# Kernel tuning notes

Measured on AMD Instinct MI355X. Metric: run time of the kernel, lower is better.

## Reference

```python
import jax, jax.numpy as jnp
import numpy as np

T = 2048; HIDDEN = 2048; HQ = 32; G = 2; D = 64
KERNEL = 32; STRIDE = 16; BLOCK = 64; TOPK = 16
INIT_BLOCKS = 1; LOCAL_BLOCKS = 2; WINDOW = 512
ROPE_BASE = 10000.0
NEG = -1e30


def _rope(x):
    # x: [T, H, D], non-interleaved rotate-half rope
    t, h, d = x.shape
    half = d // 2
    inv = 1.0 / (ROPE_BASE ** (jnp.arange(half, dtype=jnp.float32) / half))
    freqs = jnp.arange(t, dtype=jnp.float32)[:, None] * inv[None, :]
    cos = jnp.cos(freqs)[:, None, :]
    sin = jnp.sin(freqs)[:, None, :]
    x1, x2 = x[..., :half], x[..., half:]
    return jnp.concatenate([x1 * cos - x2 * sin, x2 * cos + x1 * sin], axis=-1)


def setup_inputs() -> dict:
    key = jax.random.key(0)
    ks = jax.random.split(key, 8)
    s = 0.02
    return {
        "hidden_states": jax.random.normal(ks[0], (1, T, HIDDEN), jnp.float32),
        "Wq": jax.random.normal(ks[1], (HQ * D, HIDDEN), jnp.float32) * s,
        "Wk": jax.random.normal(ks[2], (G * D, HIDDEN), jnp.float32) * s,
        "Wv": jax.random.normal(ks[3], (G * D, HIDDEN), jnp.float32) * s,
        "Wo": jax.random.normal(ks[4], (HIDDEN, HQ * D), jnp.float32) * s,
        "Wgate": jax.random.normal(ks[5], (3, HIDDEN), jnp.float32) * s,
        "compress_key": jax.random.normal(ks[6], (G, D * KERNEL, D), jnp.float32) * s,
        "compress_value": jax.random.normal(ks[7], (G, D * KERNEL, D), jnp.float32) * s,
    }


def reference(hidden_states, Wq, Wk, Wv, Wo, Wgate, compress_key, compress_value):
    x = hidden_states[0]                      # [T, HIDDEN] (single varlen sequence)
    scale = 1.0 / np.sqrt(D).astype(np.float32)
    q = (x @ Wq.T).reshape(T, HQ, D)
    k = (x @ Wk.T).reshape(T, G, D)
    v = (x @ Wv.T).reshape(T, G, D)
    gate = jax.nn.sigmoid(x @ Wgate.T)        # [T, 3]
    q = _rope(q)
    k = _rope(k)

    # --- branch 1: compressed attention (linear_compress + compressed_attention) ---
    C = (T - KERNEL) // STRIDE + 1            # compressed sequence length
    starts = jnp.arange(C) * STRIDE
    win_idx = starts[:, None] + jnp.arange(KERNEL)[None, :]        # [C, KERNEL]
    kw = k[win_idx].transpose(2, 0, 1, 3).reshape(G, C, KERNEL * D)
    vw = v[win_idx].transpose(2, 0, 1, 3).reshape(G, C, KERNEL * D)
    ck = jnp.einsum('gcf,gfd->cgd', kw, compress_key)              # [C, G, D]
    cv = jnp.einsum('gcf,gfd->cgd', vw, compress_value)

    qg = q.reshape(T, G, HQ // G, D)          # [T, G, group, D]
    cs = jnp.einsum('tghd,cgd->ghtc', qg, ck) * scale              # [G, grp, T, C]
    # query i may attend compressed token j iff i >= j*stride + kernel - 1
    cmask = jnp.arange(T)[:, None] >= (starts + KERNEL - 1)[None, :]  # [T, C]
    cs = jnp.where(cmask[None, None], cs, NEG)
    p = jax.nn.softmax(cs, axis=-1)
    valid = cmask.any(-1)                     # queries with >=1 compressed key
    p = jnp.where(valid[None, None, :, None], p, 0.0)
    comp_out = jnp.einsum('ghtc,cgd->tghd', p, cv).reshape(T, HQ, D)

    # --- topk block selection from pooled compressed attention scores ---
    NB = T // BLOCK
    bstart = jnp.arange(NB) * BLOCK
    # compressed token j overlaps key block b
    overlap = ((starts[:, None] < bstart[None, :] + BLOCK) &
               (starts[:, None] + KERNEL > bstart[None, :])).astype(p.dtype)  # [C, NB]
    score = jnp.einsum('ghtc,cb->gtb', p, overlap)                 # [G, T, NB]
    qblock = jnp.arange(T) // BLOCK
    b = jnp.arange(NB)
    causal_b = b[None, :] <= qblock[:, None]                       # [T, NB]
    forced = (b[None, :] < INIT_BLOCKS) | (((qblock[:, None] - b[None, :]) < LOCAL_BLOCKS) & causal_b)
    score = jnp.where(forced[None], jnp.inf, score)
    score = jnp.where(causal_b[None], score, -jnp.inf)
    _, topk_idx = jax.lax.top_k(score, TOPK)                       # [G, T, TOPK]
    tk_valid = jnp.take_along_axis(score, topk_idx, axis=-1) > -jnp.inf
    sel = ((topk_idx[..., None] == b) & tk_valid[..., None]).any(axis=2)  # [G, T, NB]

    # --- branch 2: topk block-sparse attention ---
    key_block = jnp.arange(T) // BLOCK
    keymask = sel[:, :, key_block]                                 # [G, T, Tk]
    causal = jnp.arange(T)[:, None] >= jnp.arange(T)[None, :]      # [T, Tk]
    smask = keymask & causal[None]
    ss = jnp.einsum('tghd,sgd->ghts', qg, k) * scale               # [G, grp, T, Tk]
    ss = jnp.where(smask[:, None], ss, NEG)
    sparse_out = jnp.einsum('ghts,sgd->tghd', jax.nn.softmax(ss, -1), v).reshape(T, HQ, D)

    # --- branch 3: sliding window attention (causal, left window) ---
    delta = jnp.arange(T)[:, None] - jnp.arange(T)[None, :]
    wmask = (delta >= 0) & (delta <= WINDOW)                       # [T, Tk]
    ws = jnp.einsum('tghd,sgd->ghts', qg, k) * scale
    ws = jnp.where(wmask[None, None], ws, NEG)
    slide_out = jnp.einsum('ghts,sgd->tghd', jax.nn.softmax(ws, -1), v).reshape(T, HQ, D)

    # --- learned gate fusion + output projection ---
    out = (gate[:, 0, None, None] * comp_out +
           gate[:, 1, None, None] * sparse_out +
           gate[:, 2, None, None] * slide_out)                    # [T, HQ, D]
    o = out.reshape(T, HQ * D) @ Wo.T
    return o[None]                                                 # [1, T, HIDDEN]
```

## Files before the change

### kernel.cpp

```cpp
#include <hip/hip_runtime.h>
#include <math.h>

#define T_SEQ 2048
#define NHQ 32
#define NG 2
#define HD 64
#define CSTRIDE 16
#define KVGW 384

typedef __attribute__((ext_vector_type(8))) short short8_t;
typedef __attribute__((ext_vector_type(4))) short short4_t;
typedef __attribute__((ext_vector_type(4))) float f32x4;

__device__ __forceinline__ ushort f2bf(float x) {
  union { float f; unsigned u; } c; c.f = x;
  unsigned r = c.u + 0x7fff + ((c.u >> 16) & 1);
  return (ushort)(r >> 16);
}
__device__ __forceinline__ float bf2f(ushort u) {
  union { unsigned u; float f; } c; c.u = ((unsigned)u) << 16;
  return c.f;
}

__device__ __forceinline__ void glds16(const ushort* g, ushort* l) {
  __builtin_amdgcn_global_load_lds(
      (const __attribute__((address_space(1))) unsigned int*)g,
      (__attribute__((address_space(3))) unsigned int*)l, 16, 0, 0);
}

__global__ __launch_bounds__(512) void mgemm(
    const ushort* __restrict__ A, const ushort* __restrict__ B,
    float* __restrict__ C, int M, int N, int K) {
  __shared__ __align__(16) ushort As[128 * 64];
  __shared__ __align__(16) ushort Bs[128 * 64];
  const int tid = threadIdx.x;
  const int lane = tid & 63, w = tid >> 6;
  const int quad = lane >> 4, l16 = lane & 15;
  const int m0 = blockIdx.y * 128, n0 = blockIdx.x * 128;
  const int mq = (w & 1) * 64, nq = (w >> 1) * 32;
  f32x4 acc[4][2];
  const f32x4 fz = {0.f, 0.f, 0.f, 0.f};
  #pragma unroll
  for (int i = 0; i < 4; ++i)
    #pragma unroll
    for (int j = 0; j < 2; ++j) acc[i][j] = fz;

  for (int k0 = 0; k0 < K; k0 += 64) {
    __syncthreads();
    #pragma unroll
    for (int j = 0; j < 2; ++j) {
      int ci = j * 512 + tid;
      int row = ci >> 3, cl = ci & 7;
      int kc = cl ^ (row & 7);
      glds16(A + ((size_t)(m0 + row) * K + k0 + kc * 8), &As[ci * 8]);
      glds16(B + ((size_t)(n0 + row) * K + k0 + kc * 8), &Bs[ci * 8]);
    }
    __syncthreads();
    #pragma unroll
    for (int kt = 0; kt < 2; ++kt) {
      short8_t af[4], bf_[2];
      #pragma unroll
      for (int mt = 0; mt < 4; ++mt) {
        int row = mq + mt * 16 + l16;
        int cl = (kt * 4 + quad) ^ (row & 7);
        af[mt] = *(const short8_t*)&As[row * 64 + cl * 8];
      }
      #pragma unroll
      for (int nt = 0; nt < 2; ++nt) {
        int row = nq + nt * 16 + l16;
        int cl = (kt * 4 + quad) ^ (row & 7);
        bf_[nt] = *(const short8_t*)&Bs[row * 64 + cl * 8];
      }
      #pragma unroll
      for (int mt = 0; mt < 4; ++mt)
        #pragma unroll
        for (int nt = 0; nt < 2; ++nt)
          acc[mt][nt] = __builtin_amdgcn_mfma_f32_16x16x32_bf16(
              af[mt], bf_[nt], acc[mt][nt], 0, 0, 0);
    }
  }
  #pragma unroll
  for (int mt = 0; mt < 4; ++mt)
    #pragma unroll
    for (int nt = 0; nt < 2; ++nt)
      #pragma unroll
      for (int r = 0; r < 4; ++r) {
        int m = m0 + mq + mt * 16 + quad * 4 + r;
        int n = n0 + nq + nt * 16 + l16;
        C[(size_t)m * N + n] = acc[mt][nt][r];
      }
}

__global__ __launch_bounds__(256) void cvt_bf(const float* __restrict__ src,
                                              ushort* __restrict__ dst, int n) {
  int i = blockIdx.x * 256 + threadIdx.x;
  if (i < n) dst[i] = f2bf(src[i]);
}

__global__ __launch_bounds__(256) void cvt_sum2_bf(const float* __restrict__ a,
                                                   const float* __restrict__ b,
                                                   ushort* __restrict__ dst, int n) {
  int i = blockIdx.x * 256 + threadIdx.x;
  if (i < n) dst[i] = f2bf(a[i] + b[i]);
}

__global__ __launch_bounds__(256) void pack_wkvg(
    const float* __restrict__ Wk, const float* __restrict__ Wv,
    const float* __restrict__ Wg, ushort* __restrict__ dst) {
  int i = blockIdx.x * 256 + threadIdx.x;
  if (i >= KVGW * 2048) return;
  int n = i >> 11, k = i & 2047;
  float v;
  if (n < 128) v = Wk[(size_t)n * 2048 + k];
  else if (n < 256) v = Wv[(size_t)(n - 128) * 2048 + k];
  else if (n < 259) v = Wg[(size_t)(n - 256) * 2048 + k];
  else v = 0.f;
  dst[i] = f2bf(v);
}

__global__ __launch_bounds__(256) void cvt_vt(const float* __restrict__ kvg,
                                              ushort* __restrict__ vt) {
  int i = blockIdx.x * 256 + threadIdx.x;
  if (i >= T_SEQ * NG * HD) return;
  int d = i & 63, g = (i >> 6) & 1, s = i >> 7;
  int blk = s >> 6, k = s & 63;
  int snew = blk * 64 + (((k >> 2) ^ (d & 15)) << 2) + (k & 3);
  vt[((size_t)g * HD + d) * T_SEQ + snew] =
      f2bf(kvg[(size_t)s * KVGW + 128 + g * 64 + d]);
}

__global__ __launch_bounds__(256) void rope_all(
    const float* __restrict__ q, float* __restrict__ kvg,
    ushort* __restrict__ qbf, ushort* __restrict__ kbf) {
  const int t = blockIdx.x;
  const float lnb_over = 9.210340371976184f / 32.f;
  for (int job = threadIdx.x; job < (NHQ + NG) * 32; job += 256) {
    int h = job >> 5, j = job & 31;
    float inv = expf(-(float)j * lnb_over);
    float fr = (float)t * inv;
    float c_ = cosf(fr), s_ = sinf(fr);
    if (h < NHQ) {
      const float cq = c_ * 0.125f, sq = s_ * 0.125f;
      const float* base = q + ((size_t)t * NHQ + h) * HD;
      float x1 = base[j], x2 = base[j + 32];
      ushort* ob = qbf + ((size_t)t * NHQ + h) * HD;
      ob[j] = f2bf(x1 * cq - x2 * sq);
      ob[j + 32] = f2bf(x2 * cq + x1 * sq);
    } else {
      int g = h - NHQ;
      float* base = kvg + (size_t)t * KVGW + g * 64;
      float x1 = base[j], x2 = base[j + 32];
      float o1 = x1 * c_ - x2 * s_, o2 = x2 * c_ + x1 * s_;
      base[j] = o1; base[j + 32] = o2;
      kbf[(size_t)t * 128 + g * 64 + j] = f2bf(o1);
      kbf[(size_t)t * 128 + g * 64 + j + 32] = f2bf(o2);
    }
  }
}

__global__ __launch_bounds__(256) void compress_kv(
    const float* __restrict__ kvg,
    const float* __restrict__ Wck, const float* __restrict__ Wcv,
    ushort* __restrict__ ck16, ushort* __restrict__ cvt16) {
  const int c = blockIdx.x, g = blockIdx.y;
  const int tid = threadIdx.x;
  if (c == 127) {
    if (tid < 64) ck16[((size_t)127 * NG + g) * HD + tid] = 0;
    else if (tid < 128) cvt16[((size_t)g * HD + (tid - 64)) * 128 + 127] = 0;
    return;
  }
  const int d = tid & 63, chunk = tid >> 6;
  __shared__ float red[2][4][64];
  float ak = 0.f, av = 0.f;
  for (int f = chunk * 512; f < chunk * 512 + 512; ++f) {
    int i = f >> 6, e = f & 63;
    int trow = c * CSTRIDE + i;
    float kv = kvg[(size_t)trow * KVGW + g * 64 + e];
    float vv = kvg[(size_t)trow * KVGW + 128 + g * 64 + e];
    ak += kv * Wck[((size_t)g * 2048 + f) * HD + d];
    av += vv * Wcv[((size_t)g * 2048 + f) * HD + d];
  }
  red[0][chunk][d] = ak;
  red[1][chunk][d] = av;
  __syncthreads();
  if (tid < 64) {
    ck16[((size_t)c * NG + g) * HD + tid] =
        f2bf(red[0][0][tid] + red[0][1][tid] + red[0][2][tid] + red[0][3][tid]);
  } else if (tid < 128) {
    int dd = tid - 64;
    cvt16[((size_t)g * HD + dd) * 128 + c] =
        f2bf(red[1][0][dd] + red[1][1][dd] + red[1][2][dd] + red[1][3][dd]);
  }
}

__global__ __launch_bounds__(512) void comp_attn(
    const ushort* __restrict__ qbf, const ushort* __restrict__ ck16,
    const ushort* __restrict__ cvt16, const float* __restrict__ kvg,
    float* __restrict__ comb, unsigned* __restrict__ sel) {
  const int tb = blockIdx.x, g = blockIdx.y;
  const int t0 = tb * 16;
  const int tid = threadIdx.x, lane = tid & 63, w = tid >> 6;
  const int quad = lane >> 4, l16 = lane & 15;
  const int qb = t0 >> 6;

  __shared__ float colsum[16][129];
  for (int i = tid; i < 16 * 129; i += 512) ((float*)colsum)[i] = 0.f;
  __syncthreads();

  const int t = t0 + l16;
  const int cmaxv = (t >= 31) ? min(126, (t - 31) >> 4) : -1;
  const int h0 = w * 2;

  short8_t qB[2][2];
  #pragma unroll
  for (int hh = 0; hh < 2; ++hh)
    #pragma unroll
    for (int kd = 0; kd < 2; ++kd)
      qB[hh][kd] = *(const short8_t*)(qbf +
          ((size_t)t * NHQ + g * 16 + h0 + hh) * HD + kd * 32 + quad * 8);

  const f32x4 fz = {0.f, 0.f, 0.f, 0.f};
  f32x4 sp[2][8];

  #pragma unroll
  for (int ct = 0; ct < 8; ++ct) {
    const ushort* kr = ck16 + ((size_t)(ct * 16 + l16) * NG + g) * HD + quad * 8;
    short8_t kA0 = *(const short8_t*)kr;
    short8_t kA1 = *(const short8_t*)(kr + 32);
    #pragma unroll
    for (int hh = 0; hh < 2; ++hh) {
      f32x4 c0 = __builtin_amdgcn_mfma_f32_16x16x32_bf16(kA0, qB[hh][0], fz, 0, 0, 0);
      sp[hh][ct] = __builtin_amdgcn_mfma_f32_16x16x32_bf16(kA1, qB[hh][1], c0, 0, 0, 0);
    }
  }

  short4_t pB[2][8];
  #pragma unroll
  for (int hh = 0; hh < 2; ++hh) {
    float mx = -INFINITY;
    #pragma unroll
    for (int ct = 0; ct < 8; ++ct)
      #pragma unroll
      for (int r = 0; r < 4; ++r) {
        int c = ct * 16 + quad * 4 + r;
        float s_ = (c <= cmaxv) ? sp[hh][ct][r] : -INFINITY;
        sp[hh][ct][r] = s_;
        mx = fmaxf(mx, s_);
      }
    mx = fmaxf(mx, __shfl_xor(mx, 16));
    mx = fmaxf(mx, __shfl_xor(mx, 32));
    if (mx == -INFINITY) mx = 0.f;
    float ls = 0.f;
    #pragma unroll
    for (int ct = 0; ct < 8; ++ct)
      #pragma unroll
      for (int r = 0; r < 4; ++r) {
        float p = __expf(sp[hh][ct][r] - mx);
        sp[hh][ct][r] = p;
        ls += p;
      }
    ls += __shfl_xor(ls, 16);
    ls += __shfl_xor(ls, 32);
    float inv = (ls > 0.f) ? 1.f / ls : 0.f;
    #pragma unroll
    for (int ct = 0; ct < 8; ++ct) {
      short4_t pk;
      #pragma unroll
      for (int r = 0; r < 4; ++r) {
        float pn = sp[hh][ct][r] * inv;
        sp[hh][ct][r] = pn;
        pk[r] = (short)f2bf(pn);
      }
      pB[hh][ct] = pk;
    }
  }

  #pragma unroll
  for (int ct = 0; ct < 8; ++ct)
    #pragma unroll
    for (int r = 0; r < 4; ++r)
      atomicAdd(&colsum[l16][ct * 16 + quad * 4 + r],
                sp[0][ct][r] + sp[1][ct][r]);

  f32x4 acc[2][4];
  #pragma unroll
  for (int hh = 0; hh < 2; ++hh)
    #pragma unroll
    for (int dt = 0; dt < 4; ++dt) acc[hh][dt] = fz;
  #pragma unroll
  for (int ct = 0; ct < 8; ++ct) {
    short4_t vA[4];
    #pragma unroll
    for (int dt = 0; dt < 4; ++dt)
      vA[dt] = *(const short4_t*)(cvt16 +
          ((size_t)g * HD + dt * 16 + l16) * 128 + ct * 16 + quad * 4);
    #pragma unroll
    for (int hh = 0; hh < 2; ++hh)
      #pragma unroll
      for (int dt = 0; dt < 4; ++dt)
        acc[hh][dt] = __builtin_amdgcn_mfma_f32_16x16x16bf16_1k(
            vA[dt], pB[hh][ct], acc[hh][dt], 0, 0, 0);
  }

  const float g0 = 1.f / (1.f + __expf(-kvg[(size_t)t * KVGW + 256]));
  #pragma unroll
  for (int hh = 0; hh < 2; ++hh)
    #pragma unroll
    for (int dt = 0; dt < 4; ++dt)
      #pragma unroll
      for (int r = 0; r < 4; ++r)
        comb[((size_t)t * NHQ + g * 16 + h0 + hh) * HD + dt * 16 + quad * 4 + r] =
            g0 * acc[hh][dt][r];

  __syncthreads();

  {
    const int tl = tid >> 5;
    const int b = tid & 31;
    float s;
    if (b > qb) s = -INFINITY;
    else if (b == 0 || qb - b < 2) s = INFINITY;
    else {
      s = 0.f;
      #pragma unroll
      for (int i = 0; i < 5; ++i) s += colsum[tl][4 * b - 1 + i];
    }
    unsigned key = (s < 0.f) ? 0u : (__float_as_uint(s) + 1u);
    unsigned msel = 0;
    for (int it = 0; it < 16; ++it) {
      unsigned long long pk =
          (((unsigned long long)key) << 6) | (unsigned)(63 - b);
      #pragma unroll
      for (int off = 16; off >= 1; off >>= 1) {
        unsigned long long o = __shfl_xor(pk, off);
        if (o > pk) pk = o;
      }
      if ((pk >> 6) == 0) break;
      int bs = 63 - (int)(pk & 63);
      msel |= 1u << bs;
      if (b == bs) key = 0;
    }
    if (b == 0) sel[(size_t)(t0 + tl) * NG + g] = msel;
  }
}

__global__ __launch_bounds__(512, 2) void mfma_attn(
    const ushort* __restrict__ qb16, const ushort* __restrict__ kb16,
    const ushort* __restrict__ vtb, const float* __restrict__ kvg,
    const unsigned* __restrict__ sel, float* __restrict__ comb1,
    float* __restrict__ comb2) {
  const int qb = blockIdx.x, g = blockIdx.y;
  const int hgp = blockIdx.z & 7, mode = blockIdx.z >> 3;
  const int tid = threadIdx.x, lane = tid & 63, w = tid >> 6;
  const int quad = lane >> 4, l16 = lane & 15;
  const int head = g * 16 + hgp * 2 + (w >> 2);
  const int t0 = qb * 64;

  __shared__ __align__(16) ushort Ks[2][64 * 64];
  __shared__ __align__(16) ushort Vs[2][64 * 64];
  __shared__ unsigned sel_s[64];

  if (tid < 64) sel_s[tid] = sel[(size_t)(t0 + tid) * NG + g];
  __syncthreads();

  const int qg = t0 + (w & 3) * 16 + l16;
  const unsigned sbq = sel_s[(w & 3) * 16 + l16];

  short8_t qB0 = *(const short8_t*)(qb16 +
      ((size_t)qg * NHQ + head) * HD + quad * 8);
  short8_t qB1 = *(const short8_t*)(qb16 +
      ((size_t)qg * NHQ + head) * HD + 32 + quad * 8);

  float m_ = -1e30f;
  f32x4 acc[4], accL;
  const f32x4 fz = {0.f, 0.f, 0.f, 0.f};
  #pragma unroll
  for (int dt = 0; dt < 4; ++dt) acc[dt] = fz;
  accL = fz;
  const short4_t onesA = {(short)0x3F80, (short)0x3F80,
                          (short)0x3F80, (short)0x3F80};

  unsigned mrem = 0; int b0 = 0, nb = 0;
  if (mode == 0) {
    unsigned uni = sel_s[lane];
    #pragma unroll
    for (int off = 32; off >= 1; off >>= 1) uni |= __shfl_xor(uni, off);
    mrem = uni;
    nb = __popc(mrem);
  } else {
    b0 = (qb > 8) ? qb - 8 : 0;
    nb = qb - b0 + 1;
  }

  #define STAGE(buf, blk)                                                     \
    {                                                                         \
      const int blk_ = (blk);                                                 \
      const int row = tid >> 3, cl = tid & 7;                                 \
      const int kck = cl ^ (row & 7);                                         \
      glds16(kb16 + (size_t)(blk_ * 64 + row) * 128 + g * 64 + kck * 8,       \
             &Ks[buf][tid * 8]);                                              \
      glds16(vtb + ((size_t)g * 64 + row) * 2048 + blk_ * 64 + cl * 8,        \
             &Vs[buf][tid * 8]);                                              \
    }

  int blkcur;
  if (mode == 0) { blkcur = __ffs(mrem) - 1; mrem &= mrem - 1; }
  else blkcur = b0;
  STAGE(0, blkcur);
  __syncthreads();

  const int e = l16 & 7;

  for (int ib = 0; ib < nb; ++ib) {
    const int cur = ib & 1;
    const int blk = blkcur;
    if (ib + 1 < nb) {
      if (mode == 0) { blkcur = __ffs(mrem) - 1; mrem &= mrem - 1; }
      else blkcur = b0 + ib + 1;
      STAGE(cur ^ 1, blkcur);
    }

    f32x4 sp[4];
    __builtin_amdgcn_s_setprio(1);
    #pragma unroll
    for (int kt = 0; kt < 4; ++kt) {
      const ushort* kr = &Ks[cur][(kt * 16 + l16) * 64];
      short8_t kA0 = *(const short8_t*)(kr + ((quad ^ e) * 8));
      short8_t kA1 = *(const short8_t*)(kr + ((quad ^ e ^ 4) * 8));
      f32x4 c = __builtin_amdgcn_mfma_f32_16x16x32_bf16(kA0, qB0, fz, 0, 0, 0);
      sp[kt] = __builtin_amdgcn_mfma_f32_16x16x32_bf16(kA1, qB1, c, 0, 0, 0);
    }
    __builtin_amdgcn_s_setprio(0);

    const bool diag = (blk == qb);
    const bool wedge = (mode == 1) && (blk == qb - 8);
    const bool selq = (mode != 0) || (((sbq >> blk) & 1u) != 0);

    float mx = -INFINITY;
    if (!diag && !wedge) {
      #pragma unroll
      for (int kt = 0; kt < 4; ++kt)
        #pragma unroll
        for (int r = 0; r < 4; ++r) {
          float s_ = selq ? sp[kt][r] : -INFINITY;
          sp[kt][r] = s_;
          mx = fmaxf(mx, s_);
        }
    } else {
      #pragma unroll
      for (int kt = 0; kt < 4; ++kt)
        #pragma unroll
        for (int r = 0; r < 4; ++r) {
          int key = blk * 64 + kt * 16 + quad * 4 + r;
          bool ok = selq && (key <= qg) && (qg - key <= 512);
          float s_ = ok ? sp[kt][r] : -INFINITY;
          sp[kt][r] = s_;
          mx = fmaxf(mx, s_);
        }
    }
    mx = fmaxf(mx, __shfl_xor(mx, 16));
    mx = fmaxf(mx, __shfl_xor(mx, 32));
    float mold = m_;
    if (!__all(mx <= mold + 8.f)) {
      float mnew = fmaxf(mold, mx);
      float alpha = __expf(mold - mnew);
      #pragma unroll
      for (int dt = 0; dt < 4; ++dt)
        #pragma unroll
        for (int r = 0; r < 4; ++r) acc[dt][r] *= alpha;
      #pragma unroll
      for (int r = 0; r < 4; ++r) accL[r] *= alpha;
      m_ = mnew;
      mold = mnew;
    }
    short4_t pB[4];
    #pragma unroll
    for (int kt = 0; kt < 4; ++kt) {
      float p0 = __expf(sp[kt][0] - mold);
      float p1 = __expf(sp[kt][1] - mold);
      float p2 = __expf(sp[kt][2] - mold);
      float p3 = __expf(sp[kt][3] - mold);
      union { unsigned u[2]; short4_t s; } pk;
      asm("v_cvt_pk_bf16_f32 %0, %1, %2" : "=v"(pk.u[0]) : "v"(p0), "v"(p1));
      asm("v_cvt_pk_bf16_f32 %0, %1, %2" : "=v"(pk.u[1]) : "v"(p2), "v"(p3));
      pB[kt] = pk.s;
    }

    __builtin_amdgcn_s_setprio(1);
    #pragma unroll
    for (int kt = 0; kt < 4; ++kt) {
      #pragma unroll
      for (int dt = 0; dt < 4; ++dt) {
        short4_t vA = *(const short4_t*)(&Vs[cur][(dt * 16 + l16) * 64 +
                                                  (((kt * 4 + quad) ^ l16) << 2)]);
        acc[dt] = __builtin_amdgcn_mfma_f32_16x16x16bf16_1k(
            vA, pB[kt], acc[dt], 0, 0, 0);
      }
      accL = __builtin_amdgcn_mfma_f32_16x16x16bf16_1k(
          onesA, pB[kt], accL, 0, 0, 0);
    }
    __builtin_amdgcn_s_setprio(0);

    __syncthreads();
  }
  #undef STAGE

  const float l_ = accL[0];
  const float c_ =
      (1.f / (1.f + __expf(-kvg[(size_t)qg * KVGW + 257 + mode]))) / l_;
  #pragma unroll
  for (int dt = 0; dt < 4; ++dt)
    #pragma unroll
    for (int r = 0; r < 4; ++r) {
      const int d = dt * 16 + quad * 4 + r;
      size_t idx = ((size_t)qg * NHQ + head) * HD + d;
      if (mode == 0) comb1[idx] += c_ * acc[dt][r];
      else           comb2[idx]  = c_ * acc[dt][r];
    }
}

extern "C" void kernel_launch(void* const* d_in, const int* in_sizes, int n_in,
                              void* d_out, int out_size, void* d_ws, size_t ws_size,
                              hipStream_t stream) {
  const float* x   = (const float*)d_in[0];
  const float* Wq  = (const float*)d_in[1];
  const float* Wk  = (const float*)d_in[2];
  const float* Wv  = (const float*)d_in[3];
  const float* Wo  = (const float*)d_in[4];
  const float* Wg  = (const float*)d_in[5];
  const float* Wck = (const float*)d_in[6];
  const float* Wcv = (const float*)d_in[7];
  float* out = (float*)d_out;
  float* ws = (float*)d_ws;

  float* qbuf   = ws;
  float* comb1  = qbuf + 4194304;
  float* kvg    = comb1 + 4194304;
  float* ckb    = kvg + 786432;
  float* cvb    = ckb + 16384;
  unsigned* sel = (unsigned*)(cvb + 16384);
  ushort* kbf   = (ushort*)(sel + 4096);
  ushort* vtb   = kbf + 262144;
  ushort* wkvgb = vtb + 262144;
  ushort* regA  = wkvgb + 786432;
  ushort* regB  = regA + 4194304;
  ushort* xb = regA;      ushort* combb = regA;
  ushort* wqb = regB;     ushort* qbf = regB;
  float* comb2 = qbuf;
  ushort* wob = (ushort*)qbuf;

  ushort* ckb16 = (ushort*)ckb;
  ushort* cvtb  = ckb16 + 16384;

  const int CV = (4194304 + 255) / 256;
  cvt_bf<<<CV, 256, 0, stream>>>(x, xb, 4194304);
  cvt_bf<<<CV, 256, 0, stream>>>(Wq, wqb, 4194304);
  pack_wkvg<<<(KVGW * 2048 + 255) / 256, 256, 0, stream>>>(Wk, Wv, Wg, wkvgb);

  mgemm<<<dim3(16, 16), 512, 0, stream>>>(xb, wqb, qbuf, 2048, 2048, 2048);
  mgemm<<<dim3(3, 16), 512, 0, stream>>>(xb, wkvgb, kvg, 2048, KVGW, 2048);

  rope_all<<<2048, 256, 0, stream>>>(qbuf, kvg, qbf, kbf);
  cvt_vt<<<(262144 + 255) / 256, 256, 0, stream>>>(kvg, vtb);
  compress_kv<<<dim3(128, 2), 256, 0, stream>>>(kvg, Wck, Wcv, ckb16, cvtb);
  comp_attn<<<dim3(128, 2), 512, 0, stream>>>(qbf, ckb16, cvtb, kvg, comb1, sel);
  mfma_attn<<<dim3(32, 2, 16), 512, 0, stream>>>(qbf, kbf, vtb, kvg, sel, comb1, comb2);

  cvt_sum2_bf<<<CV, 256, 0, stream>>>(comb1, comb2, combb, 4194304);
  cvt_bf<<<CV, 256, 0, stream>>>(Wo, wob, 4194304);
  mgemm<<<dim3(16, 16), 512, 0, stream>>>(combb, wob, out, 2048, 2048, 2048);
}
```

Before: 399.5 us.

## Shrink GEMM tile to 128x64, vectorize conversions, reverse attention block order

The GEMM kernel now uses 256-thread blocks with 128x64 output tiles, doubling the grid so more blocks fill the CUs, though each block reuses less data. The fp32-to-bf16 conversion kernels now process four elements per thread with float4 loads and short4 stores, cutting instruction count per element. Both attention kernels launch query blocks in reverse order, so the longer causal blocks start first and load balance improves. Together these are unrelated tweaks touching several kernels.

```diff
diff --git a/kernel.cpp b/kernel.cpp
--- a/kernel.cpp
+++ b/kernel.cpp
@@ -28,15 +28,15 @@
       (__attribute__((address_space(3))) unsigned int*)l, 16, 0, 0);
 }
 
-__global__ __launch_bounds__(512) void mgemm(
+__global__ __launch_bounds__(256) void mgemm(
     const ushort* __restrict__ A, const ushort* __restrict__ B,
     float* __restrict__ C, int M, int N, int K) {
   __shared__ __align__(16) ushort As[128 * 64];
-  __shared__ __align__(16) ushort Bs[128 * 64];
+  __shared__ __align__(16) ushort Bs[64 * 64];
   const int tid = threadIdx.x;
   const int lane = tid & 63, w = tid >> 6;
   const int quad = lane >> 4, l16 = lane & 15;
-  const int m0 = blockIdx.y * 128, n0 = blockIdx.x * 128;
+  const int m0 = blockIdx.y * 128, n0 = blockIdx.x * 64;
   const int mq = (w & 1) * 64, nq = (w >> 1) * 32;
   f32x4 acc[4][2];
   const f32x4 fz = {0.f, 0.f, 0.f, 0.f};
@@ -48,11 +48,17 @@
   for (int k0 = 0; k0 < K; k0 += 64) {
     __syncthreads();
     #pragma unroll
-    for (int j = 0; j < 2; ++j) {
-      int ci = j * 512 + tid;
+    for (int j = 0; j < 4; ++j) {
+      int ci = j * 256 + tid;
       int row = ci >> 3, cl = ci & 7;
       int kc = cl ^ (row & 7);
       glds16(A + ((size_t)(m0 + row) * K + k0 + kc * 8), &As[ci * 8]);
+    }
+    #pragma unroll
+    for (int j = 0; j < 2; ++j) {
+      int ci = j * 256 + tid;
+      int row = ci >> 3, cl = ci & 7;
+      int kc = cl ^ (row & 7);
       glds16(B + ((size_t)(n0 + row) * K + k0 + kc * 8), &Bs[ci * 8]);
     }
     __syncthreads();
@@ -93,15 +99,24 @@
 
 __global__ __launch_bounds__(256) void cvt_bf(const float* __restrict__ src,
                                               ushort* __restrict__ dst, int n) {
-  int i = blockIdx.x * 256 + threadIdx.x;
-  if (i < n) dst[i] = f2bf(src[i]);
+  int i = (blockIdx.x * 256 + threadIdx.x) * 4;
+  if (i >= n) return;
+  float4 v = *(const float4*)(src + i);
+  short4_t o = {(short)f2bf(v.x), (short)f2bf(v.y),
+                (short)f2bf(v.z), (short)f2bf(v.w)};
+  *(short4_t*)(dst + i) = o;
 }
 
 __global__ __launch_bounds__(256) void cvt_sum2_bf(const float* __restrict__ a,
                                                    const float* __restrict__ b,
                                                    ushort* __restrict__ dst, int n) {
-  int i = blockIdx.x * 256 + threadIdx.x;
-  if (i < n) dst[i] = f2bf(a[i] + b[i]);
+  int i = (blockIdx.x * 256 + threadIdx.x) * 4;
+  if (i >= n) return;
+  float4 va = *(const float4*)(a + i);
+  float4 vb = *(const float4*)(b + i);
+  short4_t o = {(short)f2bf(va.x + vb.x), (short)f2bf(va.y + vb.y),
+                (short)f2bf(va.z + vb.z), (short)f2bf(va.w + vb.w)};
+  *(short4_t*)(dst + i) = o;
 }
 
 __global__ __launch_bounds__(256) void pack_wkvg(
@@ -197,7 +212,7 @@
     const ushort* __restrict__ qbf, const ushort* __restrict__ ck16,
     const ushort* __restrict__ cvt16, const float* __restrict__ kvg,
     float* __restrict__ comb, unsigned* __restrict__ sel) {
-  const int tb = blockIdx.x, g = blockIdx.y;
+  const int tb = 127 - blockIdx.x, g = blockIdx.y;
   const int t0 = tb * 16;
   const int tid = threadIdx.x, lane = tid & 63, w = tid >> 6;
   const int quad = lane >> 4, l16 = lane & 15;
@@ -349,7 +364,7 @@
     const ushort* __restrict__ vtb, const float* __restrict__ kvg,
     const unsigned* __restrict__ sel, float* __restrict__ comb1,
     float* __restrict__ comb2) {
-  const int qb = blockIdx.x, g = blockIdx.y;
+  const int qb = 31 - blockIdx.x, g = blockIdx.y;
   const int hgp = blockIdx.z & 7, mode = blockIdx.z >> 3;
   const int tid = threadIdx.x, lane = tid & 63, w = tid >> 6;
   const int quad = lane >> 4, l16 = lane & 15;
@@ -552,13 +567,13 @@
   ushort* ckb16 = (ushort*)ckb;
   ushort* cvtb  = ckb16 + 16384;
 
-  const int CV = (4194304 + 255) / 256;
-  cvt_bf<<<CV, 256, 0, stream>>>(x, xb, 4194304);
-  cvt_bf<<<CV, 256, 0, stream>>>(Wq, wqb, 4194304);
+  const int CV4 = (1048576 + 255) / 256;
+  cvt_bf<<<CV4, 256, 0, stream>>>(x, xb, 4194304);
+  cvt_bf<<<CV4, 256, 0, stream>>>(Wq, wqb, 4194304);
   pack_wkvg<<<(KVGW * 2048 + 255) / 256, 256, 0, stream>>>(Wk, Wv, Wg, wkvgb);
 
-  mgemm<<<dim3(16, 16), 512, 0, stream>>>(xb, wqb, qbuf, 2048, 2048, 2048);
-  mgemm<<<dim3(3, 16), 512, 0, stream>>>(xb, wkvgb, kvg, 2048, KVGW, 2048);
+  mgemm<<<dim3(32, 16), 256, 0, stream>>>(xb, wqb, qbuf, 2048, 2048, 2048);
+  mgemm<<<dim3(6, 16), 256, 0, stream>>>(xb, wkvgb, kvg, 2048, KVGW, 2048);
 
   rope_all<<<2048, 256, 0, stream>>>(qbuf, kvg, qbf, kbf);
   cvt_vt<<<(262144 + 255) / 256, 256, 0, stream>>>(kvg, vtb);
@@ -566,7 +581,7 @@
   comp_attn<<<dim3(128, 2), 512, 0, stream>>>(qbf, ckb16, cvtb, kvg, comb1, sel);
   mfma_attn<<<dim3(32, 2, 16), 512, 0, stream>>>(qbf, kbf, vtb, kvg, sel, comb1, comb2);
 
-  cvt_sum2_bf<<<CV, 256, 0, stream>>>(comb1, comb2, combb, 4194304);
-  cvt_bf<<<CV, 256, 0, stream>>>(Wo, wob, 4194304);
-  mgemm<<<dim3(16, 16), 512, 0, stream>>>(combb, wob, out, 2048, 2048, 2048);
-}
+  cvt_sum2_bf<<<CV4, 256, 0, stream>>>(comb1, comb2, combb, 4194304);
+  cvt_bf<<<CV4, 256, 0, stream>>>(Wo, wob, 4194304);
+  mgemm<<<dim3(32, 16), 256, 0, stream>>>(combb, wob, out, 2048, 2048, 2048);
+}
```

Result: faster. 388.1 us (-2.8%).
